# Optimization experiments

Hardware: AMD Instinct MI355X
Metric: run time of the kernel (lower is better)

The kernel has to match this reference:

```python
import jax, jax.numpy as jnp
from jax import lax
import numpy as np

B, T, D, H, L, O = 64, 256, 256, 256, 50, 2


def setup_inputs() -> dict:
    key = jax.random.key(0)
    ks = jax.random.split(key, 7)
    s = 0.05  # small init to keep gates out of saturation
    return {
        "x": jax.random.normal(ks[0], (B, T, D), jnp.float32),
        "W_ih": jax.random.normal(ks[1], (L, 4 * H, H), jnp.float32) * s,
        "W_hh": jax.random.normal(ks[2], (L, 4 * H, H), jnp.float32) * s,
        "b_ih": jax.random.normal(ks[3], (L, 4 * H), jnp.float32) * s,
        "b_hh": jax.random.normal(ks[4], (L, 4 * H), jnp.float32) * s,
        "W_out": jax.random.normal(ks[5], (O, H), jnp.float32) * s,
        "b_out": jax.random.normal(ks[6], (O,), jnp.float32) * s,
    }


def _lstm_layer(x_seq, wih, whh, bih, bhh):
    # x_seq: [B, T, H_in]; PyTorch gate order i, f, g, o
    b = x_seq.shape[0]
    h = wih.shape[0] // 4
    bias = bih + bhh
    # precompute input projections for all timesteps (one big GEMM)
    xg = jnp.einsum("bti,gi->btg", x_seq, wih) + bias  # [B, T, 4H]

    def step(carry, xg_t):
        hprev, cprev = carry
        gates = xg_t + hprev @ whh.T  # [B, 4H]
        i, f, g, o = jnp.split(gates, 4, axis=-1)
        i = jax.nn.sigmoid(i)
        f = jax.nn.sigmoid(f)
        g = jnp.tanh(g)
        o = jax.nn.sigmoid(o)
        c = f * cprev + i * g
        hnew = o * jnp.tanh(c)
        return (hnew, c), hnew

    h0 = jnp.zeros((b, h), x_seq.dtype)
    (_, _), hs = lax.scan(step, (h0, h0), jnp.swapaxes(xg, 0, 1))
    return jnp.swapaxes(hs, 0, 1)  # [B, T, H]


def reference(x, W_ih, W_hh, b_ih, b_hh, W_out, b_out):
    def layer_step(carry, p):
        wih, whh, bih, bhh = p
        return _lstm_layer(carry, wih, whh, bih, bhh), None

    y, _ = lax.scan(layer_step, x, (W_ih, W_hh, b_ih, b_hh))
    logits = jnp.einsum("bth,oh->bto", y, W_out) + b_out
    return jax.nn.sigmoid(logits)
```

## Files before the change

### kernel.cpp

```cpp
#include <hip/hip_runtime.h>
#include <hip/hip_bf16.h>
#include <stdint.h>
#include <string.h>

#define NB   64
#define NT   256
#define NH   256
#define NL   50
#define NK   512
#define NG   1024

typedef __attribute__((ext_vector_type(8)))  short   short8;
typedef __attribute__((ext_vector_type(8)))  __bf16  bf16x8;
typedef __attribute__((ext_vector_type(4)))  float   float4v;
typedef __attribute__((ext_vector_type(4)))  int     int4v;

__device__ __forceinline__ unsigned short f2bf(float f) {
  union { float f; uint32_t u; } v; v.f = f;
  uint32_t u = v.u;
  uint32_t r = (u + 0x7FFFu + ((u >> 16) & 1u)) >> 16;
  return (unsigned short)r;
}
__device__ __forceinline__ float bf2f(unsigned short s) {
  union { uint32_t u; float f; } v; v.u = ((uint32_t)s) << 16;
  return v.f;
}
__device__ __forceinline__ float sigmoid_f(float x) {
  return 1.0f / (1.0f + __expf(-x));
}
__device__ __forceinline__ float tanh_f(float x) {
  float e = __expf(-2.0f * __builtin_fabsf(x));
  float r = (1.0f - e) / (1.0f + e);
  return __builtin_copysignf(r, x);
}

__device__ __forceinline__ short8 ldg_sc1_b128(const unsigned short* p) {
  short8 r;
  asm volatile("global_load_dwordx4 %0, %1, off sc1" : "=v"(r) : "v"(p) : "memory");
  return r;
}
__device__ __forceinline__ void stg_sc1_b128(unsigned short* p, short8 v) {
  asm volatile("global_store_dwordx4 %0, %1, off sc1" :: "v"(p), "v"(v) : "memory");
}
__device__ __forceinline__ void wait_vm0() {
  asm volatile("s_waitcnt vmcnt(0)" ::: "memory");
}
__device__ __forceinline__ void wave_wait_all4(const int* p) {
  for (;;) {
    int4v f;
    asm volatile("global_load_dwordx4 %0, %1, off sc1\n\ts_waitcnt vmcnt(0)"
                 : "=v"(f) : "v"(p) : "memory");
    if ((f[0] & f[1] & f[2] & f[3]) != 0) break;
  }
}

#define OFF_WSWZ  0
#define OFF_BIAS  52428800
#define OFF_XBF   52633600
#define OFF_HRING 61022208
#define OFF_Y     67575808
#define OFF_PROD  75964416
#define OFF_CONS  76169216

__global__ void prep_w(const float* __restrict__ Wih, const float* __restrict__ Whh,
                       unsigned short* __restrict__ Wswz) {
  int idx = blockIdx.x * 256 + threadIdx.x;
  int j   = idx & 7;
  int lam = (idx >> 3) & 63;
  int kt  = (idx >> 9) & 15;
  int q   = (idx >> 13) & 3;
  int c   = (idx >> 15) & 15;
  int l   = idx >> 19;
  int k   = kt * 32 + (lam >> 4) * 8 + j;
  int g   = q * 256 + c * 16 + (lam & 15);
  float v = (k < 256) ? Wih[(l * NG + g) * 256 + k]
                      : Whh[(l * NG + g) * 256 + (k - 256)];
  Wswz[idx] = f2bf(v);
}

__global__ void prep_bias(const float* __restrict__ bih, const float* __restrict__ bhh,
                          float* __restrict__ Bias) {
  int idx = blockIdx.x * 256 + threadIdx.x;
  int col = idx & 15; int q = (idx >> 4) & 3; int c = (idx >> 6) & 15; int l = idx >> 10;
  int g = q * 256 + c * 16 + col;
  Bias[idx] = bih[l * NG + g] + bhh[l * NG + g];
}

__global__ void prep_x(const float* __restrict__ x, unsigned short* __restrict__ Xbf) {
  int idx = blockIdx.x * 256 + threadIdx.x;
  int d = idx & 255; int t = (idx >> 8) & 255; int b = idx >> 16;
  Xbf[(t * NB + b) * 256 + d] = f2bf(x[idx]);
}

__global__ void zero_flags(int* __restrict__ p) {
  p[blockIdx.x * 256 + threadIdx.x] = 0;
}

#define RSTRIDE 81
#define HSTRIDE 264
__global__ __launch_bounds__(256, 1) void lstm_persistent(
    const unsigned short* __restrict__ Wswz,
    const float* __restrict__ Bias,
    const unsigned short* __restrict__ Xbf,
    unsigned short* __restrict__ Hring,
    unsigned short* __restrict__ Y,
    int* __restrict__ prod4,
    int* __restrict__ cons4) {
  int xcd = blockIdx.x & 7;
  int jj  = blockIdx.x >> 3;
  int l   = xcd * 7 + (jj >> 2);
  int w   = jj & 3;
  if (jj >= 28 || l >= NL) return;
  int tid = threadIdx.x;

  __shared__ unsigned short hc[64 * RSTRIDE * 8];
  __shared__ unsigned short hout[64 * HSTRIDE];

  int wv   = tid >> 6;
  int ln   = tid & 63;
  int c    = w * 4 + wv;
  int colg = ln & 15;
  int quad = ln >> 4;
  bool pvside = (wv & 1);
  int  brb    = wv >> 1;

  bf16x8 wreg[64];
  {
    const unsigned short* wp = Wswz + (size_t)(l * 16 + c) * 32768 + ln * 8;
#pragma unroll
    for (int i = 0; i < 64; ++i)
      wreg[i] = *(const bf16x8*)(wp + i * 512);
  }
  float bv[4];
  {
    const float* bp = Bias + l * NG + c * 64;
#pragma unroll
    for (int q = 0; q < 4; ++q) bv[q] = bp[q * 16 + colg];
  }

  float cr[4][4] = {};
  int j = c * 16 + colg;
  bool last = (l == NL - 1);

  for (int t = 0; t < NT; ++t) {
    {
      short8 v[16];
      int e  = ln & 31;
      int rs = ln >> 5;
      if (!pvside) {
        if (l > 0) wave_wait_all4(&prod4[((l - 1) * NT + t) * 4]);
        const unsigned short* In = (l == 0)
            ? (Xbf + t * (NB * 256))
            : (Hring + (((t & 3) * NL + (l - 1)) * NB) * 256);
#pragma unroll
        for (int i = 0; i < 16; ++i) {
          int b = i * 4 + brb * 2 + rs;
          v[i] = ldg_sc1_b128(In + b * 256 + e * 8);
        }
      } else if (t > 0) {
        wave_wait_all4(&prod4[(l * NT + (t - 1)) * 4]);
        const unsigned short* Pv = Hring + ((((t - 1) & 3) * NL + l) * NB) * 256;
#pragma unroll
        for (int i = 0; i < 16; ++i) {
          int b = i * 4 + brb * 2 + rs;
          v[i] = ldg_sc1_b128(Pv + b * 256 + e * 8);
        }
      } else {
#pragma unroll
        for (int i = 0; i < 16; ++i) v[i] = short8{0, 0, 0, 0, 0, 0, 0, 0};
      }
      wait_vm0();
      int kb = (pvside ? 32 : 0) + e;
#pragma unroll
      for (int i = 0; i < 16; ++i) {
        int b = i * 4 + brb * 2 + rs;
        *(short8*)(hc + (b * RSTRIDE + kb) * 8) = v[i];
      }
    }
    __syncthreads();
    if (tid == 0 && l > 0)
      __hip_atomic_store(&cons4[((l - 1) * NT + t) * 4 + w], 1,
                         __ATOMIC_RELAXED, __HIP_MEMORY_SCOPE_AGENT);

    float4v acc[4][4];
#pragma unroll
    for (int q = 0; q < 4; ++q) {
      float4v f4 = {bv[q], bv[q], bv[q], bv[q]};
#pragma unroll
      for (int m = 0; m < 4; ++m) acc[m][q] = f4;
    }
#pragma unroll
    for (int kt = 0; kt < 16; ++kt) {
      bf16x8 a[4];
#pragma unroll
      for (int m = 0; m < 4; ++m)
        a[m] = *(const bf16x8*)(hc + ((m * 16 + colg) * RSTRIDE + kt * 4 + quad) * 8);
#pragma unroll
      for (int m = 0; m < 4; ++m)
#pragma unroll
        for (int q = 0; q < 4; ++q)
          acc[m][q] = __builtin_amdgcn_mfma_f32_16x16x32_bf16(a[m], wreg[q * 16 + kt], acc[m][q], 0, 0, 0);
    }

#pragma unroll
    for (int m = 0; m < 4; ++m) {
#pragma unroll
      for (int r = 0; r < 4; ++r) {
        int b = m * 16 + quad * 4 + r;
        float gi = sigmoid_f(acc[m][0][r]);
        float gf = sigmoid_f(acc[m][1][r]);
        float gg = tanh_f(acc[m][2][r]);
        float go = sigmoid_f(acc[m][3][r]);
        float cn = gf * cr[m][r] + gi * gg;
        cr[m][r] = cn;
        float h = go * tanh_f(cn);
        hout[b * HSTRIDE + j] = f2bf(h);
      }
    }
    if (wv == 0 && !last && t >= 4) wave_wait_all4(&cons4[(l * NT + (t - 4)) * 4]);
    __syncthreads();

    {
      unsigned short* Hout = Hring + (((t & 3) * NL + l) * NB) * 256;
      unsigned short* Yout = Y + (t * NB) * 256;
#pragma unroll
      for (int pass = 0; pass < 2; ++pass) {
        int u   = pass * 256 + tid;
        int b   = u >> 3;
        int e8  = u & 7;
        int col = w * 64 + e8 * 8;
        short8 hv = *(const short8*)(hout + b * HSTRIDE + col);
        stg_sc1_b128(Hout + b * 256 + col, hv);
        if (last) *(short8*)(Yout + b * 256 + col) = hv;
      }
    }
    __syncthreads();
    if (tid == 0)
      __hip_atomic_store(&prod4[(l * NT + t) * 4 + w], 1,
                         __ATOMIC_RELAXED, __HIP_MEMORY_SCOPE_AGENT);
  }
}

__global__ void final_proj(const unsigned short* __restrict__ Y,
                           const float* __restrict__ Wout,
                           const float* __restrict__ bout,
                           float* __restrict__ out) {
  int t = blockIdx.x;
  int tid = threadIdx.x;
  int b = tid >> 1, o = tid & 1;
  const unsigned short* yrow = Y + (t * NB + b) * 256;
  const float* wr = Wout + o * 256;
  float s = bout[o];
  for (int k0 = 0; k0 < 256; k0 += 8) {
    short8 yv = *(const short8*)(yrow + k0);
#pragma unroll
    for (int e = 0; e < 8; ++e)
      s += bf2f(((unsigned short*)&yv)[e]) * wr[k0 + e];
  }
  out[(b * NT + t) * 2 + o] = 1.0f / (1.0f + __expf(-s));
}

extern "C" void kernel_launch(void* const* d_in, const int* in_sizes, int n_in,
                              void* d_out, int out_size, void* d_ws, size_t ws_size,
                              hipStream_t stream) {
  (void)in_sizes; (void)n_in; (void)out_size; (void)ws_size;
  const float* x    = (const float*)d_in[0];
  const float* Wih  = (const float*)d_in[1];
  const float* Whh  = (const float*)d_in[2];
  const float* bih  = (const float*)d_in[3];
  const float* bhh  = (const float*)d_in[4];
  const float* Wout = (const float*)d_in[5];
  const float* bout = (const float*)d_in[6];
  float* out = (float*)d_out;

  char* ws = (char*)d_ws;
  unsigned short* Wswz  = (unsigned short*)(ws + OFF_WSWZ);
  float*          Bias  = (float*)(ws + OFF_BIAS);
  unsigned short* Xbf   = (unsigned short*)(ws + OFF_XBF);
  unsigned short* Hring = (unsigned short*)(ws + OFF_HRING);
  unsigned short* Y     = (unsigned short*)(ws + OFF_Y);
  int*            prod4 = (int*)(ws + OFF_PROD);
  int*            cons4 = (int*)(ws + OFF_CONS);

  prep_w    <<<102400, 256, 0, stream>>>(Wih, Whh, Wswz);
  prep_bias <<<200,    256, 0, stream>>>(bih, bhh, Bias);
  prep_x    <<<16384,  256, 0, stream>>>(x, Xbf);
  zero_flags<<<400,    256, 0, stream>>>(prod4);

  lstm_persistent<<<256, 256, 0, stream>>>(Wswz, Bias, Xbf, Hring, Y, prod4, cons4);

  final_proj<<<NT, 128, 0, stream>>>(Y, Wout, bout, out);
}
```

Measured before the change: 2.407 ms.

## Replace block barriers with per-wave producer flags and direct scattered h stores

Each wave now computes its gates and writes h directly to the global ring with 2-byte stores, then publishes its own per-wave ready flag. Consumers poll 16 flags with a ballot, backing off with s_sleep. This removes the LDS staging of h and two block-wide barriers per timestep, shortening the serial dependency chain between layers. The cost is many small uncoalesced stores, a larger flag array, and more polling traffic.

```diff
diff --git a/kernel.cpp b/kernel.cpp
--- a/kernel.cpp
+++ b/kernel.cpp
@@ -13,7 +13,6 @@
 typedef __attribute__((ext_vector_type(8)))  short   short8;
 typedef __attribute__((ext_vector_type(8)))  __bf16  bf16x8;
 typedef __attribute__((ext_vector_type(4)))  float   float4v;
-typedef __attribute__((ext_vector_type(4)))  int     int4v;
 
 __device__ __forceinline__ unsigned short f2bf(float f) {
   union { float f; uint32_t u; } v; v.f = f;
@@ -39,18 +38,30 @@
   asm volatile("global_load_dwordx4 %0, %1, off sc1" : "=v"(r) : "v"(p) : "memory");
   return r;
 }
-__device__ __forceinline__ void stg_sc1_b128(unsigned short* p, short8 v) {
-  asm volatile("global_store_dwordx4 %0, %1, off sc1" :: "v"(p), "v"(v) : "memory");
+__device__ __forceinline__ void stg_sc1_b16(unsigned short* p, int v) {
+  asm volatile("global_store_short %0, %1, off sc1" :: "v"(p), "v"(v) : "memory");
 }
 __device__ __forceinline__ void wait_vm0() {
   asm volatile("s_waitcnt vmcnt(0)" ::: "memory");
 }
-__device__ __forceinline__ void wave_wait_all4(const int* p) {
+__device__ __forceinline__ void wave_wait16(const int* p, int ln) {
+  const int* a = p + (ln & 15);
   for (;;) {
-    int4v f;
-    asm volatile("global_load_dwordx4 %0, %1, off sc1\n\ts_waitcnt vmcnt(0)"
-                 : "=v"(f) : "v"(p) : "memory");
-    if ((f[0] & f[1] & f[2] & f[3]) != 0) break;
+    int f;
+    asm volatile("global_load_dword %0, %1, off sc1\n\ts_waitcnt vmcnt(0)"
+                 : "=v"(f) : "v"(a) : "memory");
+    if (__ballot(f != 0) == ~0ull) break;
+    __builtin_amdgcn_s_sleep(1);
+  }
+}
+__device__ __forceinline__ void wave_wait4(const int* p, int ln) {
+  const int* a = p + (ln & 3);
+  for (;;) {
+    int f;
+    asm volatile("global_load_dword %0, %1, off sc1\n\ts_waitcnt vmcnt(0)"
+                 : "=v"(f) : "v"(a) : "memory");
+    if (__ballot(f != 0) == ~0ull) break;
+    __builtin_amdgcn_s_sleep(1);
   }
 }
 
@@ -60,7 +71,7 @@
 #define OFF_HRING 61022208
 #define OFF_Y     67575808
 #define OFF_PROD  75964416
-#define OFF_CONS  76169216
+#define OFF_CONS  76783616
 
 __global__ void prep_w(const float* __restrict__ Wih, const float* __restrict__ Whh,
                        unsigned short* __restrict__ Wswz) {
@@ -97,14 +108,13 @@
 }
 
 #define RSTRIDE 81
-#define HSTRIDE 264
 __global__ __launch_bounds__(256, 1) void lstm_persistent(
     const unsigned short* __restrict__ Wswz,
     const float* __restrict__ Bias,
     const unsigned short* __restrict__ Xbf,
     unsigned short* __restrict__ Hring,
     unsigned short* __restrict__ Y,
-    int* __restrict__ prod4,
+    int* __restrict__ prod16,
     int* __restrict__ cons4) {
   int xcd = blockIdx.x & 7;
   int jj  = blockIdx.x >> 3;
@@ -114,7 +124,6 @@
   int tid = threadIdx.x;
 
   __shared__ unsigned short hc[64 * RSTRIDE * 8];
-  __shared__ unsigned short hout[64 * HSTRIDE];
 
   int wv   = tid >> 6;
   int ln   = tid & 63;
@@ -143,22 +152,29 @@
   bool last = (l == NL - 1);
 
   for (int t = 0; t < NT; ++t) {
+    short8 v[16];
     {
-      short8 v[16];
       int e  = ln & 31;
       int rs = ln >> 5;
       if (!pvside) {
-        if (l > 0) wave_wait_all4(&prod4[((l - 1) * NT + t) * 4]);
-        const unsigned short* In = (l == 0)
-            ? (Xbf + t * (NB * 256))
-            : (Hring + (((t & 3) * NL + (l - 1)) * NB) * 256);
-#pragma unroll
-        for (int i = 0; i < 16; ++i) {
-          int b = i * 4 + brb * 2 + rs;
-          v[i] = ldg_sc1_b128(In + b * 256 + e * 8);
+        if (l > 0) {
+          wave_wait16(&prod16[((l - 1) * NT + t) * 16], ln);
+          const unsigned short* In = Hring + (((t & 3) * NL + (l - 1)) * NB) * 256;
+#pragma unroll
+          for (int i = 0; i < 16; ++i) {
+            int b = i * 4 + brb * 2 + rs;
+            v[i] = ldg_sc1_b128(In + b * 256 + e * 8);
+          }
+        } else {
+          const unsigned short* In = Xbf + t * (NB * 256);
+#pragma unroll
+          for (int i = 0; i < 16; ++i) {
+            int b = i * 4 + brb * 2 + rs;
+            v[i] = *(const short8*)(In + b * 256 + e * 8);
+          }
         }
       } else if (t > 0) {
-        wave_wait_all4(&prod4[(l * NT + (t - 1)) * 4]);
+        wave_wait16(&prod16[(l * NT + (t - 1)) * 16], ln);
         const unsigned short* Pv = Hring + ((((t - 1) & 3) * NL + l) * NB) * 256;
 #pragma unroll
         for (int i = 0; i < 16; ++i) {
@@ -170,6 +186,11 @@
         for (int i = 0; i < 16; ++i) v[i] = short8{0, 0, 0, 0, 0, 0, 0, 0};
       }
       wait_vm0();
+    }
+    __syncthreads();
+    {
+      int e  = ln & 31;
+      int rs = ln >> 5;
       int kb = (pvside ? 32 : 0) + e;
 #pragma unroll
       for (int i = 0; i < 16; ++i) {
@@ -202,42 +223,33 @@
           acc[m][q] = __builtin_amdgcn_mfma_f32_16x16x32_bf16(a[m], wreg[q * 16 + kt], acc[m][q], 0, 0, 0);
     }
 
-#pragma unroll
-    for (int m = 0; m < 4; ++m) {
-#pragma unroll
-      for (int r = 0; r < 4; ++r) {
-        int b = m * 16 + quad * 4 + r;
-        float gi = sigmoid_f(acc[m][0][r]);
-        float gf = sigmoid_f(acc[m][1][r]);
-        float gg = tanh_f(acc[m][2][r]);
-        float go = sigmoid_f(acc[m][3][r]);
-        float cn = gf * cr[m][r] + gi * gg;
-        cr[m][r] = cn;
-        float h = go * tanh_f(cn);
-        hout[b * HSTRIDE + j] = f2bf(h);
-      }
-    }
-    if (wv == 0 && !last && t >= 4) wave_wait_all4(&cons4[(l * NT + (t - 4)) * 4]);
-    __syncthreads();
+    if (!last && t >= 4) wave_wait4(&cons4[(l * NT + (t - 4)) * 4], ln);
 
     {
       unsigned short* Hout = Hring + (((t & 3) * NL + l) * NB) * 256;
       unsigned short* Yout = Y + (t * NB) * 256;
 #pragma unroll
-      for (int pass = 0; pass < 2; ++pass) {
-        int u   = pass * 256 + tid;
-        int b   = u >> 3;
-        int e8  = u & 7;
-        int col = w * 64 + e8 * 8;
-        short8 hv = *(const short8*)(hout + b * HSTRIDE + col);
-        stg_sc1_b128(Hout + b * 256 + col, hv);
-        if (last) *(short8*)(Yout + b * 256 + col) = hv;
+      for (int m = 0; m < 4; ++m) {
+#pragma unroll
+        for (int r = 0; r < 4; ++r) {
+          int b = m * 16 + quad * 4 + r;
+          float gi = sigmoid_f(acc[m][0][r]);
+          float gf = sigmoid_f(acc[m][1][r]);
+          float gg = tanh_f(acc[m][2][r]);
+          float go = sigmoid_f(acc[m][3][r]);
+          float cn = gf * cr[m][r] + gi * gg;
+          cr[m][r] = cn;
+          float h = go * tanh_f(cn);
+          unsigned short hb = f2bf(h);
+          stg_sc1_b16(Hout + b * 256 + j, (int)hb);
+          if (last) Yout[b * 256 + j] = hb;
+        }
       }
-    }
-    __syncthreads();
-    if (tid == 0)
-      __hip_atomic_store(&prod4[(l * NT + t) * 4 + w], 1,
-                         __ATOMIC_RELAXED, __HIP_MEMORY_SCOPE_AGENT);
+      wait_vm0();
+      if (ln == 0)
+        __hip_atomic_store(&prod16[(l * NT + t) * 16 + c], 1,
+                           __ATOMIC_RELAXED, __HIP_MEMORY_SCOPE_AGENT);
+    }
   }
 }
 
@@ -274,20 +286,20 @@
   float* out = (float*)d_out;
 
   char* ws = (char*)d_ws;
-  unsigned short* Wswz  = (unsigned short*)(ws + OFF_WSWZ);
-  float*          Bias  = (float*)(ws + OFF_BIAS);
-  unsigned short* Xbf   = (unsigned short*)(ws + OFF_XBF);
-  unsigned short* Hring = (unsigned short*)(ws + OFF_HRING);
-  unsigned short* Y     = (unsigned short*)(ws + OFF_Y);
-  int*            prod4 = (int*)(ws + OFF_PROD);
-  int*            cons4 = (int*)(ws + OFF_CONS);
+  unsigned short* Wswz   = (unsigned short*)(ws + OFF_WSWZ);
+  float*          Bias   = (float*)(ws + OFF_BIAS);
+  unsigned short* Xbf    = (unsigned short*)(ws + OFF_XBF);
+  unsigned short* Hring  = (unsigned short*)(ws + OFF_HRING);
+  unsigned short* Y      = (unsigned short*)(ws + OFF_Y);
+  int*            prod16 = (int*)(ws + OFF_PROD);
+  int*            cons4  = (int*)(ws + OFF_CONS);
 
   prep_w    <<<102400, 256, 0, stream>>>(Wih, Whh, Wswz);
   prep_bias <<<200,    256, 0, stream>>>(bih, bhh, Bias);
   prep_x    <<<16384,  256, 0, stream>>>(x, Xbf);
-  zero_flags<<<400,    256, 0, stream>>>(prod4);
-
-  lstm_persistent<<<256, 256, 0, stream>>>(Wswz, Bias, Xbf, Hring, Y, prod4, cons4);
+  zero_flags<<<1000,   256, 0, stream>>>(prod16);
+
+  lstm_persistent<<<256, 256, 0, stream>>>(Wswz, Bias, Xbf, Hring, Y, prod16, cons4);
 
   final_proj<<<NT, 128, 0, stream>>>(Y, Wout, bout, out);
 }
```

After: 3.914 ms. 1.63x slower.
